# Optimization experiments

Hardware: AMD Instinct MI355X
Metric: run time of the kernel (lower is better)

## Reference

```python
import jax, jax.numpy as jnp
import numpy as np


def _freq_downsample(x, sf):
    # torch: stack(chunk(dim=2), 4) -> cat(chunk(dim=3), 4) -> mean(-1) -> repeat(1,1,sf,sf)
    # equivalent: mean over the sf x sf grid of contiguous blocks, then tile back.
    B, C, H, W = x.shape
    m = x.reshape(B, C, sf, H // sf, sf, W // sf).mean(axis=(2, 4))
    return jnp.tile(m, (1, 1, sf, sf))


def setup_inputs() -> dict:
    key = jax.random.key(0)
    k1, k2, k3 = jax.random.split(key, 3)
    shape = (4, 3, 256, 256)
    return {
        "STy": jax.random.normal(k1, shape, dtype=jnp.float32),
        "Fk_real": jax.random.normal(k2, shape, dtype=jnp.float32),
        "Fk_imag": jax.random.normal(k3, shape, dtype=jnp.float32),
        "sf": 2,
    }


def _forward(STy, Fk_real, Fk_imag, sf, num_iters=50, alpha=1e-6, gam=0.1):
    fft2 = lambda a: jnp.fft.fft2(a, axes=(-2, -1))
    ifft2 = lambda a: jnp.fft.ifft2(a, axes=(-2, -1))

    Fk = jax.lax.complex(Fk_real, Fk_imag)          # complex64 OTF
    FkC = jnp.conj(Fk)
    Fk2 = Fk_real ** 2 + Fk_imag ** 2               # |Fk|^2, real

    FSTy = fft2(STy)
    Fr = FkC * FSTy / (_freq_downsample(Fk2, sf) + alpha)
    pred = ifft2(Fr).real

    # finite-difference stencils DH = [1,-1] horizontal, DV vertical
    DH = jnp.zeros_like(pred).at[..., 0, 0].set(1.0).at[..., 0, 1].set(-1.0)
    DV = jnp.zeros_like(pred).at[..., 0, 0].set(1.0).at[..., 1, 0].set(-1.0)
    FDH, FDV = fft2(DH), fft2(DV)
    FDHC, FDVC = jnp.conj(FDH), jnp.conj(FDV)
    FD2 = jnp.abs(FDV) ** 2 + jnp.abs(FDH) ** 2 + 1e-8  # real

    # loop-invariant terms (identical math to recomputing each iteration)
    den = _freq_downsample(Fk2 / FD2, sf) + alpha
    FkFSTy = FkC * FSTy

    def body(carry, k):
        pred, x_old, t_old, U1, U2, D1, D2 = carry
        gam_k = gam * jnp.exp2(-k / num_iters)      # gam * 0.5 ** (k/num_iters)
        Fr = FkFSTy + alpha * (FDHC * fft2(U1 - D1) + FDVC * fft2(U2 - D2))
        Fr = (Fr - FkC * _freq_downsample(Fk * Fr / FD2, sf) / den) / (alpha * FD2)
        x_new = ifft2(Fr).real
        t_new = (1.0 + jnp.sqrt(1.0 + 4.0 * t_old ** 2)) / 2.0
        pred = x_new + (t_old - 1.0) / t_new * (x_new - x_old)
        DHr = ifft2(Fr * FDH).real
        DVr = ifft2(Fr * FDV).real
        NU1, NU2 = DHr + D1, DVr + D2
        NU = jnp.sqrt(NU1 ** 2 + NU2 ** 2 + 1e-8)
        A = jnp.maximum(0.0, NU - gam_k) + 1e-8
        A = A / (A + gam_k)                         # soft-threshold magnitude shrink
        U1n, U2n = A * NU1, A * NU2
        return (pred, x_new, t_new, U1n, U2n, D1 + DHr - U1n, D2 + DVr - U2n), None

    carry0 = (pred, pred, jnp.float32(1.0), pred, pred,
              jnp.zeros_like(pred), jnp.zeros_like(pred))
    ks = jnp.arange(num_iters, dtype=jnp.float32)
    (pred, *_), _ = jax.lax.scan(body, carry0, ks)
    return pred


def reference(STy, Fk_real, Fk_imag, sf):
    return _forward(STy, Fk_real, Fk_imag, sf)
```

## Files before the change

### kernel.cpp

```cpp
#include <hip/hip_runtime.h>
#include <math.h>

#define NIMG 12
#define NSZ 256
#define HWSZ 65536
#define NBLK 768

__device__ __forceinline__ float2 ld8(const float2* p)
{
  unsigned long long v = __hip_atomic_load((unsigned long long*)p, __ATOMIC_RELAXED,
                                           __HIP_MEMORY_SCOPE_AGENT);
  union { unsigned long long u; float2 f; } cv; cv.u = v; return cv.f;
}
__device__ __forceinline__ void st8(float2* p, float2 x)
{
  union { unsigned long long u; float2 f; } cv; cv.f = x;
  __hip_atomic_store((unsigned long long*)p, cv.u, __ATOMIC_RELAXED, __HIP_MEMORY_SCOPE_AGENT);
}
__device__ __forceinline__ float ld4(const float* p)
{
  unsigned v = __hip_atomic_load((unsigned*)p, __ATOMIC_RELAXED, __HIP_MEMORY_SCOPE_AGENT);
  union { unsigned u; float f; } cv; cv.u = v; return cv.f;
}
__device__ __forceinline__ void st4(float* p, float x)
{
  union { unsigned u; float f; } cv; cv.f = x;
  __hip_atomic_store((unsigned*)p, cv.u, __ATOMIC_RELAXED, __HIP_MEMORY_SCOPE_AGENT);
}

__device__ __forceinline__ size_t widx(int n, int u, int j)
{
  int tile = (j & 127) >> 1;
  int slot = (j & 1) + ((j >> 7) << 1);
  return ((((size_t)n << 6) + tile) << 10) + ((size_t)u << 2) + slot;
}

__device__ __forceinline__ void isync(unsigned* flags, int base, int sr, unsigned gen)
{
  asm volatile("s_waitcnt vmcnt(0)" ::: "memory");
  __syncthreads();
  int t = threadIdx.x;
  if (t < 64) {
    if (t == 0)
      __hip_atomic_store(&flags[base + sr], gen, __ATOMIC_RELAXED, __HIP_MEMORY_SCOPE_AGENT);
    unsigned v;
    int it = 0;
    do {
      if (it++ > 2) __builtin_amdgcn_s_sleep(2);
      v = __hip_atomic_load(&flags[base + t], __ATOMIC_RELAXED, __HIP_MEMORY_SCOPE_AGENT);
    } while (__any(v < gen));
  }
  __syncthreads();
  asm volatile("" ::: "memory");
}

__device__ __forceinline__ void r4_bfly(const float2* __restrict__ S, float2* __restrict__ D,
                                        int b, int m, float2 w1, float2 w2, float2 w3,
                                        float dir, bool usetw)
{
  int k = b & (m - 1);
  int base = ((b - k) << 2) + k;
  float2 x0 = S[b], x1 = S[b + 64], x2 = S[b + 128], x3 = S[b + 192];
  float t0x = x0.x + x2.x, t0y = x0.y + x2.y;
  float t1x = x0.x - x2.x, t1y = x0.y - x2.y;
  float t2x = x1.x + x3.x, t2y = x1.y + x3.y;
  float e3x = x1.x - x3.x, e3y = x1.y - x3.y;
  float t3x = -dir * e3y, t3y = dir * e3x;
  D[base] = make_float2(t0x + t2x, t0y + t2y);
  float y1x = t1x + t3x, y1y = t1y + t3y;
  float y2x = t0x - t2x, y2y = t0y - t2y;
  float y3x = t1x - t3x, y3y = t1y - t3y;
  if (usetw) {
    float w1i = dir * w1.y, w2i = dir * w2.y, w3i = dir * w3.y;
    D[base + m]     = make_float2(y1x * w1.x - y1y * w1i, y1x * w1i + y1y * w1.x);
    D[base + 2 * m] = make_float2(y2x * w2.x - y2y * w2i, y2x * w2i + y2y * w2.x);
    D[base + 3 * m] = make_float2(y3x * w3.x - y3y * w3i, y3x * w3i + y3y * w3.x);
  } else {
    D[base + m]     = make_float2(y1x, y1y);
    D[base + 2 * m] = make_float2(y2x, y2y);
    D[base + 3 * m] = make_float2(y3x, y3y);
  }
}

struct Tw { float2 a1, a2, a3, b1, b2, b3, c1, c2, c3; };

__device__ __forceinline__ float2 mktw(int q)
{
  float s, c;
  sincospif((float)q * (1.0f / 128.0f), &s, &c);
  return make_float2(c, s);
}

__device__ __forceinline__ void fft4_row(float2* A, float2* B, int lane, float dir, const Tw& tw)
{
  r4_bfly(A, B, lane, 1,  tw.a1, tw.a2, tw.a3, dir, true);
  r4_bfly(B, A, lane, 4,  tw.b1, tw.b2, tw.b3, dir, true);
  r4_bfly(A, B, lane, 16, tw.c1, tw.c2, tw.c3, dir, true);
  r4_bfly(B, A, lane, 64, tw.a1, tw.a1, tw.a1, dir, false);
}

__global__ __launch_bounds__(256, 3) void k_mega(const float* __restrict__ sty,
                                                 const float* __restrict__ fkr,
                                                 const float* __restrict__ fki,
                                                 float2* __restrict__ WG,
                                                 float2* __restrict__ WF,
                                                 float* __restrict__ Dh,
                                                 float* __restrict__ x49,
                                                 float* __restrict__ out,
                                                 float cmom, unsigned* flags)
{
  __shared__ __align__(16) float2 bufA[6][256];
  __shared__ __align__(16) float2 scrB[6][256];
  __shared__ float2 fkL[4][256];
  __shared__ float2 kfL[4][256];
  __shared__ float  dnL[256];
  __shared__ float  D1L[4][256];
  __shared__ float  D2L[4][256];

  float*   aL   = (float*)scrB;
  float*   bL   = ((float*)scrB) + 5 * 256;
  double2* Ml   = (double2*)scrB;
  float*   dsAp = (float*)scrB;

  int t = threadIdx.x;
  int slot = ((blockIdx.x & 7) * 96) + (blockIdx.x >> 3);
  int n = slot >> 6;
  int sr = slot & 63;
  int fbase = n << 6;
  int r0 = sr << 2;
  int j0 = sr << 1;
  int w = t >> 6, lane = t & 63;
  const float sc = 1.0f / 65536.0f;
  size_t cb = ((((size_t)n << 6) + sr) << 10);
  unsigned gen = 0;

  Tw tw;
  {
    int qa = lane, qb = lane & ~3, qc = lane & ~15;
    tw.a1 = mktw(qa);  tw.a2 = mktw(2 * qa); tw.a3 = mktw(3 * qa);
    tw.b1 = mktw(qb);  tw.b2 = mktw(2 * qb); tw.b3 = mktw(3 * qb);
    tw.c1 = mktw(qc);  tw.c2 = mktw(2 * qc); tw.c3 = mktw(3 * qc);
  }
  int u0 = t & 127, pp = t >> 7;
  double fdgc[4], rM[4], rF[4];
  double rdn0, rdn1;
  {
    double s;
    s = sinpi((double)u0 * (1.0 / 256.0));         double fdu0 = 4.0 * s * s;
    s = sinpi((double)(u0 + 128) * (1.0 / 256.0)); double fdu1 = 4.0 * s * s;
#pragma unroll
    for (int c = 0; c < 4; ++c) {
      int gc = j0 + (c & 1) + ((c >> 1) << 7);
      s = sinpi((double)gc * (1.0 / 256.0));
      fdgc[c] = 4.0 * s * s;
    }
#pragma unroll
    for (int s4 = 0; s4 < 4; ++s4) {
      double fdu = (s4 & 1) ? fdu1 : fdu0;
      rM[s4] = 1.0 / (fdu + fdgc[pp + ((s4 >> 1) << 1)] + 1e-8);
    }
    double fdt = pp ? fdu1 : fdu0;
#pragma unroll
    for (int c = 0; c < 4; ++c) rF[c] = 1.0 / (fdt + fdgc[c] + 1e-8);
  }

  {
    const float* src = sty + (size_t)n * HWSZ + (size_t)(r0 + w) * NSZ;
#pragma unroll
    for (int q = 0; q < 4; ++q) { int j = lane + (q << 6); bufA[w][j] = make_float2(src[j], 0.f); }
    fft4_row(bufA[w], scrB[w], lane, -1.f, tw);
#pragma unroll
    for (int q = 0; q < 4; ++q) { int j = lane + (q << 6); st8(&WG[widx(n, r0 + w, j)], bufA[w][j]); }
#pragma unroll
    for (int c = 0; c < 4; ++c) {
      int gc = j0 + (c & 1) + ((c >> 1) << 7);
      size_t idx = (size_t)n * HWSZ + (size_t)t * NSZ + gc;
      fkL[c][t] = make_float2(fkr[idx], fki[idx]);
    }
  }
  isync(flags, fbase, sr, ++gen);

  {
#pragma unroll
    for (int q = 0; q < 4; ++q) { int u = lane + (q << 6); bufA[w][u] = ld8(&WG[cb + (u << 2) + w]); }
    fft4_row(bufA[w], scrB[w], lane, -1.f, tw);
    __syncthreads();
#pragma unroll
    for (int c = 0; c < 4; ++c) {
      float2 K = fkL[c][t];
      float2 f = bufA[c][t];
      kfL[c][t] = make_float2(K.x * f.x + K.y * f.y, K.x * f.y - K.y * f.x);
    }
    {
      double s1 = 0.0, s2 = 0.0;
#pragma unroll
      for (int s4 = 0; s4 < 4; ++s4) {
        int u = u0 + ((s4 & 1) << 7);
        int c = pp + ((s4 >> 1) << 1);
        double kr = fkL[c][u].x, ki = fkL[c][u].y;
        double k2 = kr * kr + ki * ki;
        s1 += k2;
        s2 += k2 * rM[s4];
      }
      dnL[u0 * 2 + pp] = (float)(s2 * 0.25 + 1e-6);
      dsAp[pp * 128 + u0] = (float)(s1 * 0.25 + 1e-6);
    }
    __syncthreads();
    rdn0 = 1.0 / (double)dnL[u0 * 2];
    rdn1 = 1.0 / (double)dnL[u0 * 2 + 1];
#pragma unroll
    for (int c = 0; c < 4; ++c) {
      float d = dsAp[(c & 1) * 128 + u0];
      float2 kf = kfL[c][t];
      bufA[c][t] = make_float2(kf.x / d, kf.y / d);
    }
    __syncthreads();
    fft4_row(bufA[w], scrB[w], lane, +1.f, tw);
#pragma unroll
    for (int q = 0; q < 4; ++q) { int u = lane + (q << 6); st8(&WF[cb + (u << 2) + w], bufA[w][u]); }
  }
  isync(flags, fbase, sr, ++gen);

  for (int k = 0; k < 50; ++k) {
    float gamp = (k >= 1) ? (float)(0.1 * exp2(-(double)(k - 1) / 50.0)) : 0.f;

    {
      int gr = (r0 + w - 1) & 255;
#pragma unroll
      for (int q = 0; q < 4; ++q) { int j = lane + (q << 6); bufA[w][j] = ld8(&WF[widx(n, gr, j)]); }
      fft4_row(bufA[w], scrB[w], lane, +1.f, tw);
      if (w < 2) {
        int e = 4 + w;
        int gr2 = (r0 + e - 1) & 255;
#pragma unroll
        for (int q = 0; q < 4; ++q) { int j = lane + (q << 6); bufA[e][j] = ld8(&WF[widx(n, gr2, j)]); }
        fft4_row(bufA[e], scrB[e], lane, +1.f, tw);
      }
    }
    __syncthreads();
    {
      int jm1 = (t - 1) & 255;
      size_t hR = (((size_t)n << 6) + ((sr + 1) & 63)) << 9;
      size_t hW = (((size_t)n << 6) + sr) << 9;
      const float* DhP = Dh + (size_t)((k + 1) & 1) * (NBLK * 512);
      float* DhW = Dh + (size_t)(k & 1) * (NBLK * 512);
      for (int e = 1; e <= 5; ++e) {
        int gr = (r0 + e - 1) & 255;
        float xc = bufA[e][t].x * sc;
        if (k == 49 && e <= 4) x49[(size_t)n * HWSZ + (size_t)gr * NSZ + t] = xc;
        float a, b;
        if (k == 0) {
          a = xc; b = xc;
          if (e <= 4) { D1L[e - 1][t] = 0.f; D2L[e - 1][t] = 0.f; }
        } else {
          float dhr = xc - bufA[e][jm1].x * sc;
          float dvr = xc - bufA[e - 1][t].x * sc;
          float d1, d2;
          if (e <= 4) { d1 = D1L[e - 1][t]; d2 = D2L[e - 1][t]; }
          else        { d1 = ld4(&DhP[hR + t]); d2 = ld4(&DhP[hR + 256 + t]); }
          float nu1 = dhr + d1, nu2 = dvr + d2;
          float nu = sqrtf(nu1 * nu1 + nu2 * nu2 + 1e-8f);
          float A = fmaxf(0.f, nu - gamp) + 1e-8f;
          A = A / (A + gamp);
          float u1 = A * nu1, u2 = A * nu2;
          float d1v = d1 + dhr - u1;
          float d2v = d2 + dvr - u2;
          if (e <= 4) { D1L[e - 1][t] = d1v; D2L[e - 1][t] = d2v; }
          if (e == 1) { st4(&DhW[hW + t], d1v); st4(&DhW[hW + 256 + t], d2v); }
          a = u1 - d1v; b = u2 - d2v;
        }
        aL[(e - 1) * 256 + t] = a;
        bL[(e - 1) * 256 + t] = b;
      }
    }
    __syncthreads();
    {
#pragma unroll
      for (int q = 0; q < 4; ++q) {
        int j = lane + (q << 6);
        int jp1 = (j + 1) & 255;
        float g = aL[w * 256 + j] - aL[w * 256 + jp1] + bL[w * 256 + j] - bL[(w + 1) * 256 + j];
        bufA[w][j] = make_float2(g, 0.f);
      }
      fft4_row(bufA[w], scrB[w], lane, -1.f, tw);
#pragma unroll
      for (int q = 0; q < 4; ++q) { int j = lane + (q << 6); st8(&WG[widx(n, r0 + w, j)], bufA[w][j]); }
    }
    isync(flags, fbase, sr, ++gen);

    {
#pragma unroll
      for (int q = 0; q < 4; ++q) { int u = lane + (q << 6); bufA[w][u] = ld8(&WG[cb + (u << 2) + w]); }
      fft4_row(bufA[w], scrB[w], lane, -1.f, tw);
      __syncthreads();
#pragma unroll
      for (int c = 0; c < 4; ++c) {
        float2 kf = kfL[c][t];
        float2 fg = bufA[c][t];
        bufA[c][t] = make_float2(kf.x + 1e-6f * fg.x, kf.y + 1e-6f * fg.y);
      }
      __syncthreads();
      {
        double sx = 0.0, sy = 0.0;
#pragma unroll
        for (int s4 = 0; s4 < 4; ++s4) {
          int u = u0 + ((s4 & 1) << 7);
          int c = pp + ((s4 >> 1) << 1);
          float2 f1 = bufA[c][u];
          double kr = fkL[c][u].x, ki = fkL[c][u].y;
          sx += (kr * (double)f1.x - ki * (double)f1.y) * rM[s4];
          sy += (kr * (double)f1.y + ki * (double)f1.x) * rM[s4];
        }
        Ml[pp * 128 + u0] = make_double2(sx * 0.25, sy * 0.25);
      }
      __syncthreads();
#pragma unroll
      for (int c = 0; c < 4; ++c) {
        float2 f1 = bufA[c][t];
        double2 m = Ml[(c & 1) * 128 + u0];
        double rden = (c & 1) ? rdn1 : rdn0;
        double kr = fkL[c][t].x, ki = fkL[c][t].y;
        double px = (kr * m.x + ki * m.y) * rden;
        double py = (kr * m.y - ki * m.x) * rden;
        double s2 = 1e6 * rF[c];
        bufA[c][t] = make_float2((float)(((double)f1.x - px) * s2),
                                 (float)(((double)f1.y - py) * s2));
      }
      __syncthreads();
      fft4_row(bufA[w], scrB[w], lane, +1.f, tw);
#pragma unroll
      for (int q = 0; q < 4; ++q) { int u = lane + (q << 6); st8(&WF[cb + (u << 2) + w], bufA[w][u]); }
    }
    isync(flags, fbase, sr, ++gen);
  }

  {
    int gr = r0 + w;
#pragma unroll
    for (int q = 0; q < 4; ++q) { int j = lane + (q << 6); bufA[w][j] = ld8(&WF[widx(n, gr, j)]); }
    fft4_row(bufA[w], scrB[w], lane, +1.f, tw);
    size_t base = (size_t)n * HWSZ + (size_t)gr * NSZ;
#pragma unroll
    for (int q = 0; q < 4; ++q) {
      int j = lane + (q << 6);
      float v = bufA[w][j].x * sc;
      out[base + j] = v + cmom * (v - x49[base + j]);
    }
  }
}

__device__ __forceinline__ void fft256g(float2* A, float2* B, const float2* twl, int lane,
                                        float dir, bool active)
{
  float2* src = A;
  float2* dst = B;
  int m = 1;
#pragma unroll
  for (int s = 0; s < 8; ++s) {
    __syncthreads();
    if (active) {
#pragma unroll
      for (int h = 0; h < 2; ++h) {
        int b = lane + (h << 6);
        int k = b & (m - 1);
        int jm = b - k;
        float2 a = src[b];
        float2 c = src[b + 128];
        float2 wv = twl[jm];
        float wr = wv.x, wi = dir * wv.y;
        float ex = a.x - c.x, ey = a.y - c.y;
        dst[2 * jm + k]     = make_float2(a.x + c.x, a.y + c.y);
        dst[2 * jm + k + m] = make_float2(ex * wr - ey * wi, ex * wi + ey * wr);
      }
    }
    float2* t = src; src = dst; dst = t;
    m <<= 1;
  }
  __syncthreads();
}
__device__ __forceinline__ void fft256(float2* A, float2* B, const float2* twl, int lane, float dir)
{
  fft256g(A, B, twl, lane, dir, true);
}
__device__ __forceinline__ void make_tw(float2* twl, int t)
{
  float s, c;
  sincospif((float)t * (1.0f / 128.0f), &s, &c);
  twl[t] = make_float2(c, s);
}
__device__ __forceinline__ double fdval(const float2* twl, int k)
{
  return 2.0 - 2.0 * (double)twl[k].x;
}

__global__ __launch_bounds__(256) void k_rowfwd_sty(const float* __restrict__ sty,
                                                    float2* __restrict__ Wb)
{
  __shared__ float2 twl[256];
  __shared__ float2 bufA[4][256];
  __shared__ float2 bufB[4][256];
  int t = threadIdx.x;
  make_tw(twl, t);
  int n = blockIdx.x >> 6;
  int r0 = (blockIdx.x & 63) << 2;
  int w = t >> 6, lane = t & 63;
  const float* src = sty + (size_t)n * HWSZ + (size_t)(r0 + w) * NSZ;
#pragma unroll
  for (int q = 0; q < 4; ++q) { int j = lane + (q << 6); bufA[w][j] = make_float2(src[j], 0.f); }
  fft256(bufA[w], bufB[w], twl, lane, -1.f);
  float2* dst = Wb + (size_t)n * HWSZ + (size_t)(r0 + w) * NSZ;
#pragma unroll
  for (int q = 0; q < 4; ++q) { int j = lane + (q << 6); dst[j] = bufA[w][j]; }
}

__global__ __launch_bounds__(256) void k_colsetup(float2* __restrict__ Wb,
                                                  float2* __restrict__ FkF,
                                                  const float* __restrict__ fkr,
                                                  const float* __restrict__ fki,
                                                  float* __restrict__ denq)
{
  __shared__ float2 twl[256];
  __shared__ float2 bufA[4][256];
  __shared__ float2 bufB[4][256];
  __shared__ float dsA[2][128];
  int t = threadIdx.x;
  make_tw(twl, t);
  int n = blockIdx.x >> 6;
  int j0 = (blockIdx.x & 63) << 1;
  int w = t >> 6, lane = t & 63;
  int gcw = j0 + (w & 1) + ((w >> 1) << 7);
  float2* Wn = Wb + (size_t)n * HWSZ;
#pragma unroll
  for (int q = 0; q < 4; ++q) { int u = lane + (q << 6); bufA[w][u] = Wn[(size_t)u * NSZ + gcw]; }
  fft256(bufA[w], bufB[w], twl, lane, -1.f);
#pragma unroll
  for (int c = 0; c < 4; ++c) {
    int u = t;
    int gc = j0 + (c & 1) + ((c >> 1) << 7);
    size_t idx = (size_t)n * HWSZ + (size_t)u * NSZ + gc;
    float kr = fkr[idx], ki = fki[idx];
    float2 f = bufA[c][u];
    float2 kf = make_float2(kr * f.x + ki * f.y, kr * f.y - ki * f.x);
    FkF[idx] = kf;
    bufA[c][u] = kf;
  }
  __syncthreads();
  {
    int u0 = t & 127, p = t >> 7;
    double s1 = 0.0, s2 = 0.0;
#pragma unroll
    for (int s = 0; s < 4; ++s) {
      int u = u0 + ((s & 1) << 7);
      int c = p + ((s >> 1) << 1);
      int gc = j0 + (c & 1) + ((c >> 1) << 7);
      size_t idx = (size_t)n * HWSZ + (size_t)u * NSZ + gc;
      double kr = fkr[idx], ki = fki[idx];
      double k2 = kr * kr + ki * ki;
      double fd2 = fdval(twl, u) + fdval(twl, gc) + 1e-8;
      s1 += k2;
      s2 += k2 / fd2;
    }
    denq[(size_t)n * 16384 + (size_t)u0 * 128 + (j0 + p)] = (float)(s2 * 0.25 + 1e-6);
    dsA[p][u0] = (float)(s1 * 0.25 + 1e-6);
  }
  __syncthreads();
#pragma unroll
  for (int c = 0; c < 4; ++c) {
    int u = t;
    float d = dsA[c & 1][u & 127];
    float2 kf = bufA[c][u];
    bufA[c][u] = make_float2(kf.x / d, kf.y / d);
  }
  fft256(bufA[w], bufB[w], twl, lane, +1.f);
#pragma unroll
  for (int q = 0; q < 4; ++q) { int u = lane + (q << 6); Wn[(size_t)u * NSZ + gcw] = bufA[w][u]; }
}

__global__ __launch_bounds__(256) void k_spatial_rowfwd(const float* __restrict__ x,
                                                        const float* __restrict__ D1p,
                                                        const float* __restrict__ D2p,
                                                        float* __restrict__ D1n,
                                                        float* __restrict__ D2n,
                                                        float2* __restrict__ Wb,
                                                        float gamp, int firstIter)
{
  __shared__ float2 twl[256];
  __shared__ float aL[5][256];
  __shared__ float bL[5][256];
  __shared__ float2 bufA[4][256];
  __shared__ float2 bufB[4][256];
  int t = threadIdx.x;
  make_tw(twl, t);
  int n = blockIdx.x >> 6;
  int r0 = (blockIdx.x & 63) << 2;
  const float* xn = x + (size_t)n * HWSZ;
  for (int rr = 0; rr < 5; ++rr) {
    int i = (r0 + rr) & 255;
    int im1 = (i - 1) & 255;
    int j = t;
    int jm1 = (j - 1) & 255;
    float xc = xn[(size_t)i * NSZ + j];
    float a, b;
    if (firstIter) {
      a = xc; b = xc;
    } else {
      float dhr = xc - xn[(size_t)i * NSZ + jm1];
      float dvr = xc - xn[(size_t)im1 * NSZ + j];
      size_t idx = (size_t)n * HWSZ + (size_t)i * NSZ + j;
      float d1 = D1p[idx], d2 = D2p[idx];
      float nu1 = dhr + d1, nu2 = dvr + d2;
      float nu = sqrtf(nu1 * nu1 + nu2 * nu2 + 1e-8f);
      float A = fmaxf(0.f, nu - gamp) + 1e-8f;
      A = A / (A + gamp);
      float u1 = A * nu1, u2 = A * nu2;
      float d1v = d1 + dhr - u1;
      float d2v = d2 + dvr - u2;
      if (rr < 4) { D1n[idx] = d1v; D2n[idx] = d2v; }
      a = u1 - d1v; b = u2 - d2v;
    }
    aL[rr][j] = a;
    bL[rr][j] = b;
  }
  __syncthreads();
  int w = t >> 6, lane = t & 63;
#pragma unroll
  for (int q = 0; q < 4; ++q) {
    int j = lane + (q << 6);
    int jp1 = (j + 1) & 255;
    float g = aL[w][j] - aL[w][jp1] + bL[w][j] - bL[w + 1][j];
    bufA[w][j] = make_float2(g, 0.f);
  }
  fft256(bufA[w], bufB[w], twl, lane, -1.f);
  float2* dst = Wb + (size_t)n * HWSZ + (size_t)(r0 + w) * NSZ;
#pragma unroll
  for (int q = 0; q < 4; ++q) { int j = lane + (q << 6); dst[j] = bufA[w][j]; }
}

__global__ __launch_bounds__(256) void k_colphase(float2* __restrict__ Wb,
                                                  const float2* __restrict__ FkF,
                                                  const float* __restrict__ fkr,
                                                  const float* __restrict__ fki,
                                                  const float* __restrict__ denq)
{
  __shared__ float2 twl[256];
  __shared__ float2 bufA[4][256];
  __shared__ float2 bufB[4][256];
  __shared__ double2 Mll[2][128];
  int t = threadIdx.x;
  make_tw(twl, t);
  int n = blockIdx.x >> 6;
  int j0 = (blockIdx.x & 63) << 1;
  int w = t >> 6, lane = t & 63;
  int gcw = j0 + (w & 1) + ((w >> 1) << 7);
  float2* Wn = Wb + (size_t)n * HWSZ;
#pragma unroll
  for (int q = 0; q < 4; ++q) { int u = lane + (q << 6); bufA[w][u] = Wn[(size_t)u * NSZ + gcw]; }
  fft256(bufA[w], bufB[w], twl, lane, -1.f);
#pragma unroll
  for (int c = 0; c < 4; ++c) {
    int u = t;
    int gc = j0 + (c & 1) + ((c >> 1) << 7);
    size_t idx = (size_t)n * HWSZ + (size_t)u * NSZ + gc;
    float2 kf = FkF[idx];
    float2 fg = bufA[c][u];
    bufA[c][u] = make_float2(kf.x + 1e-6f * fg.x, kf.y + 1e-6f * fg.y);
  }
  __syncthreads();
  {
    int u0 = t & 127, p = t >> 7;
    double sx = 0.0, sy = 0.0;
#pragma unroll
    for (int s = 0; s < 4; ++s) {
      int u = u0 + ((s & 1) << 7);
      int c = p + ((s >> 1) << 1);
      int gc = j0 + (c & 1) + ((c >> 1) << 7);
      size_t idx = (size_t)n * HWSZ + (size_t)u * NSZ + gc;
      float2 f1 = bufA[c][u];
      double kr = fkr[idx], ki = fki[idx];
      double fd2 = fdval(twl, u) + fdval(twl, gc) + 1e-8;
      sx += (kr * (double)f1.x - ki * (double)f1.y) / fd2;
      sy += (kr * (double)f1.y + ki * (double)f1.x) / fd2;
    }
    Mll[p][u0] = make_double2(sx * 0.25, sy * 0.25);
  }
  __syncthreads();
#pragma unroll
  for (int c = 0; c < 4; ++c) {
    int u = t;
    int gc = j0 + (c & 1) + ((c >> 1) << 7);
    size_t idx = (size_t)n * HWSZ + (size_t)u * NSZ + gc;
    float2 f1 = bufA[c][u];
    double2 m = Mll[c & 1][u & 127];
    double den = (double)denq[(size_t)n * 16384 + (size_t)(u & 127) * 128 + (j0 + (c & 1))];
    double kr = fkr[idx], ki = fki[idx];
    double px = (kr * m.x + ki * m.y) / den;
    double py = (kr * m.y - ki * m.x) / den;
    double fd2 = fdval(twl, u) + fdval(twl, gc) + 1e-8;
    double s2 = 1.0 / (1e-6 * fd2);
    bufA[c][u] = make_float2((float)(((double)f1.x - px) * s2),
                             (float)(((double)f1.y - py) * s2));
  }
  fft256(bufA[w], bufB[w], twl, lane, +1.f);
#pragma unroll
  for (int q = 0; q < 4; ++q) { int u = lane + (q << 6); Wn[(size_t)u * NSZ + gcw] = bufA[w][u]; }
}

__global__ __launch_bounds__(256) void k_rowinv(const float2* __restrict__ Wb,
                                                float* __restrict__ xout,
                                                const float* __restrict__ xold,
                                                float* __restrict__ pred,
                                                float cmom, int isLast)
{
  __shared__ float2 twl[256];
  __shared__ float2 bufA[4][256];
  __shared__ float2 bufB[4][256];
  int t = threadIdx.x;
  make_tw(twl, t);
  int n = blockIdx.x >> 6;
  int r0 = (blockIdx.x & 63) << 2;
  int w = t >> 6, lane = t & 63;
  const float2* src = Wb + (size_t)n * HWSZ + (size_t)(r0 + w) * NSZ;
#pragma unroll
  for (int q = 0; q < 4; ++q) { int j = lane + (q << 6); bufA[w][j] = src[j]; }
  fft256(bufA[w], bufB[w], twl, lane, +1.f);
  size_t base = (size_t)n * HWSZ + (size_t)(r0 + w) * NSZ;
#pragma unroll
  for (int q = 0; q < 4; ++q) {
    int j = lane + (q << 6);
    float v = bufA[w][j].x * (1.0f / 65536.0f);
    xout[base + j] = v;
    if (isLast) pred[base + j] = v + cmom * (v - xold[base + j]);
  }
}

extern "C" void kernel_launch(void* const* d_in, const int* in_sizes, int n_in,
                              void* d_out, int out_size, void* d_ws, size_t ws_size,
                              hipStream_t stream)
{
  (void)in_sizes; (void)n_in; (void)out_size; (void)ws_size;
  const float* STy = (const float*)d_in[0];
  const float* fkr = (const float*)d_in[1];
  const float* fki = (const float*)d_in[2];
  float* out = (float*)d_out;

  char* p = (char*)d_ws;
  const size_t cplx = (size_t)NIMG * HWSZ * sizeof(float2);
  const size_t realb = (size_t)NIMG * HWSZ * sizeof(float);
  float2* WG  = (float2*)p; p += cplx;
  float2* WF  = (float2*)p; p += cplx;
  float2* FkF = (float2*)p; p += cplx;
  float* denq = (float*)p;  p += (size_t)NIMG * 16384 * sizeof(float);
  float* D1a = (float*)p;   p += realb;
  float* D2a = (float*)p;   p += realb;
  float* D1b = (float*)p;   p += realb;
  float* D2b = (float*)p;   p += realb;
  float* xA  = (float*)p;   p += realb;
  float* xB  = (float*)p;   p += realb;
  float* Dh  = (float*)p;   p += (size_t)2 * NBLK * 512 * sizeof(float);
  unsigned* flags = (unsigned*)p; p += 4096;

  double t_old = 1.0, cm = 0.0;
  for (int k = 0; k < 50; ++k) {
    double t_new = (1.0 + sqrt(1.0 + 4.0 * t_old * t_old)) * 0.5;
    if (k == 49) cm = (t_old - 1.0) / t_new;
    t_old = t_new;
  }

  int maxb = 0;
  hipError_t oe = hipOccupancyMaxActiveBlocksPerMultiprocessor(&maxb, k_mega, 256, 0);
  bool coop = (oe == hipSuccess && maxb >= 3);

  dim3 grid(NBLK), blk(256);
  if (coop) {
    hipMemsetAsync(Dh, 0, (size_t)2 * NBLK * 512 * sizeof(float), stream);
    hipMemsetAsync(flags, 0, 4096, stream);
    k_mega<<<grid, blk, 0, stream>>>(STy, fkr, fki, WG, WF, Dh, xA, out, (float)cm, flags);
  } else {
    hipMemsetAsync(D1a, 0, 2 * realb, stream);
    float2* Wb = WG;
    float* x0 = xA; float* x1 = xB;
    k_rowfwd_sty<<<grid, blk, 0, stream>>>(STy, Wb);
    k_colsetup<<<grid, blk, 0, stream>>>(Wb, FkF, fkr, fki, denq);
    k_rowinv<<<grid, blk, 0, stream>>>(Wb, x0, x0, out, 0.f, 0);
    double to = 1.0;
    for (int k = 0; k < 50; ++k) {
      float gamp = (k >= 1) ? (float)(0.1 * exp2(-(double)(k - 1) / 50.0)) : 0.f;
      const float* xk = (k & 1) ? x1 : x0;
      float* xn = (k & 1) ? x0 : x1;
      const float* D1p = (k & 1) ? D1a : D1b;
      const float* D2p = (k & 1) ? D2a : D2b;
      float* D1w = (k & 1) ? D1b : D1a;
      float* D2w = (k & 1) ? D2b : D2a;
      k_spatial_rowfwd<<<grid, blk, 0, stream>>>(xk, D1p, D2p, D1w, D2w, Wb, gamp, (k == 0) ? 1 : 0);
      k_colphase<<<grid, blk, 0, stream>>>(Wb, FkF, fkr, fki, denq);
      double tn = (1.0 + sqrt(1.0 + 4.0 * to * to)) * 0.5;
      int isLast = (k == 49) ? 1 : 0;
      float cmom = (float)((to - 1.0) / tn);
      k_rowinv<<<grid, blk, 0, stream>>>(Wb, xn, xk, out, isLast ? cmom : 0.f, isLast);
      to = tn;
    }
  }
}
```

Baseline: 2.494 ms.

## Pack real-signal row FFTs in pairs and pad sync flags to separate lines

Row inverse FFTs of real outputs are now computed two at a time by packing two rows into one complex transform (a + i·b), so three waves handle six rows instead of six separate transforms. The forward row FFTs of the real gradient field are likewise paired, and the two spectra are separated using conjugate symmetry. Each sync flag is also padded to its own 128-byte slot so that blocks polling flags do not contend on shared cache lines. In exchange, fewer waves are active during the FFT phases and there is some extra arithmetic and shared-memory traffic to unpack the two spectra.

```diff
diff --git a/kernel.cpp b/kernel.cpp
--- a/kernel.cpp
+++ b/kernel.cpp
@@ -35,19 +35,21 @@
   return ((((size_t)n << 6) + tile) << 10) + ((size_t)u << 2) + slot;
 }
 
-__device__ __forceinline__ void isync(unsigned* flags, int base, int sr, unsigned gen)
+__device__ __forceinline__ void isync(unsigned* flags, int fbase, int sr, unsigned gen)
 {
   asm volatile("s_waitcnt vmcnt(0)" ::: "memory");
   __syncthreads();
   int t = threadIdx.x;
   if (t < 64) {
     if (t == 0)
-      __hip_atomic_store(&flags[base + sr], gen, __ATOMIC_RELAXED, __HIP_MEMORY_SCOPE_AGENT);
+      __hip_atomic_store(&flags[(unsigned)(fbase + sr) << 5], gen, __ATOMIC_RELAXED,
+                         __HIP_MEMORY_SCOPE_AGENT);
     unsigned v;
     int it = 0;
     do {
       if (it++ > 2) __builtin_amdgcn_s_sleep(2);
-      v = __hip_atomic_load(&flags[base + t], __ATOMIC_RELAXED, __HIP_MEMORY_SCOPE_AGENT);
+      v = __hip_atomic_load(&flags[(unsigned)(fbase + t) << 5], __ATOMIC_RELAXED,
+                            __HIP_MEMORY_SCOPE_AGENT);
     } while (__any(v < gen));
   }
   __syncthreads();
@@ -109,18 +111,17 @@
                                                  float* __restrict__ out,
                                                  float cmom, unsigned* flags)
 {
-  __shared__ __align__(16) float2 bufA[6][256];
-  __shared__ __align__(16) float2 scrB[6][256];
+  __shared__ __align__(16) float2 xw[6][256];
+  __shared__ __align__(16) float2 sw[6][256];
   __shared__ float2 fkL[4][256];
   __shared__ float2 kfL[4][256];
   __shared__ float  dnL[256];
   __shared__ float  D1L[4][256];
   __shared__ float  D2L[4][256];
 
-  float*   aL   = (float*)scrB;
-  float*   bL   = ((float*)scrB) + 5 * 256;
-  double2* Ml   = (double2*)scrB;
-  float*   dsAp = (float*)scrB;
+  float*   swf  = (float*)sw;
+  double2* Ml   = (double2*)sw;
+  float*   dsAp = (float*)sw;
 
   int t = threadIdx.x;
   int slot = ((blockIdx.x & 7) * 96) + (blockIdx.x >> 3);
@@ -167,10 +168,10 @@
   {
     const float* src = sty + (size_t)n * HWSZ + (size_t)(r0 + w) * NSZ;
 #pragma unroll
-    for (int q = 0; q < 4; ++q) { int j = lane + (q << 6); bufA[w][j] = make_float2(src[j], 0.f); }
-    fft4_row(bufA[w], scrB[w], lane, -1.f, tw);
-#pragma unroll
-    for (int q = 0; q < 4; ++q) { int j = lane + (q << 6); st8(&WG[widx(n, r0 + w, j)], bufA[w][j]); }
+    for (int q = 0; q < 4; ++q) { int j = lane + (q << 6); xw[w][j] = make_float2(src[j], 0.f); }
+    fft4_row(xw[w], sw[w], lane, -1.f, tw);
+#pragma unroll
+    for (int q = 0; q < 4; ++q) { int j = lane + (q << 6); st8(&WG[widx(n, r0 + w, j)], xw[w][j]); }
 #pragma unroll
     for (int c = 0; c < 4; ++c) {
       int gc = j0 + (c & 1) + ((c >> 1) << 7);
@@ -182,13 +183,13 @@
 
   {
 #pragma unroll
-    for (int q = 0; q < 4; ++q) { int u = lane + (q << 6); bufA[w][u] = ld8(&WG[cb + (u << 2) + w]); }
-    fft4_row(bufA[w], scrB[w], lane, -1.f, tw);
+    for (int q = 0; q < 4; ++q) { int u = lane + (q << 6); xw[w][u] = ld8(&WG[cb + (u << 2) + w]); }
+    fft4_row(xw[w], sw[w], lane, -1.f, tw);
     __syncthreads();
 #pragma unroll
     for (int c = 0; c < 4; ++c) {
       float2 K = fkL[c][t];
-      float2 f = bufA[c][t];
+      float2 f = xw[c][t];
       kfL[c][t] = make_float2(K.x * f.x + K.y * f.y, K.x * f.y - K.y * f.x);
     }
     {
@@ -212,33 +213,34 @@
     for (int c = 0; c < 4; ++c) {
       float d = dsAp[(c & 1) * 128 + u0];
       float2 kf = kfL[c][t];
-      bufA[c][t] = make_float2(kf.x / d, kf.y / d);
+      xw[c][t] = make_float2(kf.x / d, kf.y / d);
     }
     __syncthreads();
-    fft4_row(bufA[w], scrB[w], lane, +1.f, tw);
-#pragma unroll
-    for (int q = 0; q < 4; ++q) { int u = lane + (q << 6); st8(&WF[cb + (u << 2) + w], bufA[w][u]); }
+    fft4_row(xw[w], sw[w], lane, +1.f, tw);
+#pragma unroll
+    for (int q = 0; q < 4; ++q) { int u = lane + (q << 6); st8(&WF[cb + (u << 2) + w], xw[w][u]); }
   }
   isync(flags, fbase, sr, ++gen);
 
   for (int k = 0; k < 50; ++k) {
     float gamp = (k >= 1) ? (float)(0.1 * exp2(-(double)(k - 1) / 50.0)) : 0.f;
 
-    {
-      int gr = (r0 + w - 1) & 255;
-#pragma unroll
-      for (int q = 0; q < 4; ++q) { int j = lane + (q << 6); bufA[w][j] = ld8(&WF[widx(n, gr, j)]); }
-      fft4_row(bufA[w], scrB[w], lane, +1.f, tw);
-      if (w < 2) {
-        int e = 4 + w;
-        int gr2 = (r0 + e - 1) & 255;
-#pragma unroll
-        for (int q = 0; q < 4; ++q) { int j = lane + (q << 6); bufA[e][j] = ld8(&WF[widx(n, gr2, j)]); }
-        fft4_row(bufA[e], scrB[e], lane, +1.f, tw);
-      }
+    if (w < 3) {
+      int grA = (r0 + 2 * w - 1) & 255;
+      int grB = (r0 + 2 * w) & 255;
+#pragma unroll
+      for (int q = 0; q < 4; ++q) {
+        int j = lane + (q << 6);
+        float2 a = ld8(&WF[widx(n, grA, j)]);
+        float2 b = ld8(&WF[widx(n, grB, j)]);
+        xw[w][j] = make_float2(a.x - b.y, a.y + b.x);
+      }
+      fft4_row(xw[w], sw[w + 3], lane, +1.f, tw);
     }
     __syncthreads();
     {
+      float* aL = swf;
+      float* bL = swf + 1280;
       int jm1 = (t - 1) & 255;
       size_t hR = (((size_t)n << 6) + ((sr + 1) & 63)) << 9;
       size_t hW = (((size_t)n << 6) + sr) << 9;
@@ -246,15 +248,20 @@
       float* DhW = Dh + (size_t)(k & 1) * (NBLK * 512);
       for (int e = 1; e <= 5; ++e) {
         int gr = (r0 + e - 1) & 255;
-        float xc = bufA[e][t].x * sc;
+        float2 pc = xw[e >> 1][t];
+        float xc = ((e & 1) ? pc.y : pc.x) * sc;
         if (k == 49 && e <= 4) x49[(size_t)n * HWSZ + (size_t)gr * NSZ + t] = xc;
         float a, b;
         if (k == 0) {
           a = xc; b = xc;
           if (e <= 4) { D1L[e - 1][t] = 0.f; D2L[e - 1][t] = 0.f; }
         } else {
-          float dhr = xc - bufA[e][jm1].x * sc;
-          float dvr = xc - bufA[e - 1][t].x * sc;
+          float2 pl = xw[e >> 1][jm1];
+          float xl = ((e & 1) ? pl.y : pl.x) * sc;
+          float2 pu = xw[(e - 1) >> 1][t];
+          float xu = (((e - 1) & 1) ? pu.y : pu.x) * sc;
+          float dhr = xc - xl;
+          float dvr = xc - xu;
           float d1, d2;
           if (e <= 4) { d1 = D1L[e - 1][t]; d2 = D2L[e - 1][t]; }
           else        { d1 = ld4(&DhP[hR + t]); d2 = ld4(&DhP[hR + 256 + t]); }
@@ -274,30 +281,43 @@
       }
     }
     __syncthreads();
-    {
+    if (w < 2) {
+      float* aL = swf;
+      float* bL = swf + 1280;
+      int ra = 2 * w, rb = 2 * w + 1;
 #pragma unroll
       for (int q = 0; q < 4; ++q) {
         int j = lane + (q << 6);
         int jp1 = (j + 1) & 255;
-        float g = aL[w * 256 + j] - aL[w * 256 + jp1] + bL[w * 256 + j] - bL[(w + 1) * 256 + j];
-        bufA[w][j] = make_float2(g, 0.f);
-      }
-      fft4_row(bufA[w], scrB[w], lane, -1.f, tw);
-#pragma unroll
-      for (int q = 0; q < 4; ++q) { int j = lane + (q << 6); st8(&WG[widx(n, r0 + w, j)], bufA[w][j]); }
+        float g0 = aL[ra * 256 + j] - aL[ra * 256 + jp1] + bL[ra * 256 + j] - bL[(ra + 1) * 256 + j];
+        float g1 = aL[rb * 256 + j] - aL[rb * 256 + jp1] + bL[rb * 256 + j] - bL[(rb + 1) * 256 + j];
+        xw[w][j] = make_float2(g0, g1);
+      }
+      fft4_row(xw[w], xw[w + 2], lane, -1.f, tw);
+      int r1 = r0 + ra, r2 = r0 + rb;
+#pragma unroll
+      for (int q = 0; q < 4; ++q) {
+        int j = lane + (q << 6);
+        int jm = (256 - j) & 255;
+        float2 Zj = xw[w][j], Zm = xw[w][jm];
+        float2 A  = make_float2((Zj.x + Zm.x) * 0.5f, (Zj.y - Zm.y) * 0.5f);
+        float2 Bc = make_float2((Zj.y + Zm.y) * 0.5f, (Zm.x - Zj.x) * 0.5f);
+        st8(&WG[widx(n, r1, j)], A);
+        st8(&WG[widx(n, r2, j)], Bc);
+      }
     }
     isync(flags, fbase, sr, ++gen);
 
     {
 #pragma unroll
-      for (int q = 0; q < 4; ++q) { int u = lane + (q << 6); bufA[w][u] = ld8(&WG[cb + (u << 2) + w]); }
-      fft4_row(bufA[w], scrB[w], lane, -1.f, tw);
+      for (int q = 0; q < 4; ++q) { int u = lane + (q << 6); xw[w][u] = ld8(&WG[cb + (u << 2) + w]); }
+      fft4_row(xw[w], sw[w], lane, -1.f, tw);
       __syncthreads();
 #pragma unroll
       for (int c = 0; c < 4; ++c) {
         float2 kf = kfL[c][t];
-        float2 fg = bufA[c][t];
-        bufA[c][t] = make_float2(kf.x + 1e-6f * fg.x, kf.y + 1e-6f * fg.y);
+        float2 fg = xw[c][t];
+        xw[c][t] = make_float2(kf.x + 1e-6f * fg.x, kf.y + 1e-6f * fg.y);
       }
       __syncthreads();
       {
@@ -306,7 +326,7 @@
         for (int s4 = 0; s4 < 4; ++s4) {
           int u = u0 + ((s4 & 1) << 7);
           int c = pp + ((s4 >> 1) << 1);
-          float2 f1 = bufA[c][u];
+          float2 f1 = xw[c][u];
           double kr = fkL[c][u].x, ki = fkL[c][u].y;
           sx += (kr * (double)f1.x - ki * (double)f1.y) * rM[s4];
           sy += (kr * (double)f1.y + ki * (double)f1.x) * rM[s4];
@@ -316,20 +336,20 @@
       __syncthreads();
 #pragma unroll
       for (int c = 0; c < 4; ++c) {
-        float2 f1 = bufA[c][t];
+        float2 f1 = xw[c][t];
         double2 m = Ml[(c & 1) * 128 + u0];
         double rden = (c & 1) ? rdn1 : rdn0;
         double kr = fkL[c][t].x, ki = fkL[c][t].y;
         double px = (kr * m.x + ki * m.y) * rden;
         double py = (kr * m.y - ki * m.x) * rden;
         double s2 = 1e6 * rF[c];
-        bufA[c][t] = make_float2((float)(((double)f1.x - px) * s2),
-                                 (float)(((double)f1.y - py) * s2));
+        xw[c][t] = make_float2((float)(((double)f1.x - px) * s2),
+                               (float)(((double)f1.y - py) * s2));
       }
       __syncthreads();
-      fft4_row(bufA[w], scrB[w], lane, +1.f, tw);
-#pragma unroll
-      for (int q = 0; q < 4; ++q) { int u = lane + (q << 6); st8(&WF[cb + (u << 2) + w], bufA[w][u]); }
+      fft4_row(xw[w], sw[w], lane, +1.f, tw);
+#pragma unroll
+      for (int q = 0; q < 4; ++q) { int u = lane + (q << 6); st8(&WF[cb + (u << 2) + w], xw[w][u]); }
     }
     isync(flags, fbase, sr, ++gen);
   }
@@ -337,13 +357,13 @@
   {
     int gr = r0 + w;
 #pragma unroll
-    for (int q = 0; q < 4; ++q) { int j = lane + (q << 6); bufA[w][j] = ld8(&WF[widx(n, gr, j)]); }
-    fft4_row(bufA[w], scrB[w], lane, +1.f, tw);
+    for (int q = 0; q < 4; ++q) { int j = lane + (q << 6); xw[w][j] = ld8(&WF[widx(n, gr, j)]); }
+    fft4_row(xw[w], sw[w], lane, +1.f, tw);
     size_t base = (size_t)n * HWSZ + (size_t)gr * NSZ;
 #pragma unroll
     for (int q = 0; q < 4; ++q) {
       int j = lane + (q << 6);
-      float v = bufA[w][j].x * sc;
+      float v = xw[w][j].x * sc;
       out[base + j] = v + cmom * (v - x49[base + j]);
     }
   }
@@ -657,7 +677,7 @@
   float* xA  = (float*)p;   p += realb;
   float* xB  = (float*)p;   p += realb;
   float* Dh  = (float*)p;   p += (size_t)2 * NBLK * 512 * sizeof(float);
-  unsigned* flags = (unsigned*)p; p += 4096;
+  unsigned* flags = (unsigned*)p; p += (size_t)NBLK * 32 * sizeof(unsigned);
 
   double t_old = 1.0, cm = 0.0;
   for (int k = 0; k < 50; ++k) {
@@ -673,7 +693,7 @@
   dim3 grid(NBLK), blk(256);
   if (coop) {
     hipMemsetAsync(Dh, 0, (size_t)2 * NBLK * 512 * sizeof(float), stream);
-    hipMemsetAsync(flags, 0, 4096, stream);
+    hipMemsetAsync(flags, 0, (size_t)NBLK * 32 * sizeof(unsigned), stream);
     k_mega<<<grid, blk, 0, stream>>>(STy, fkr, fki, WG, WF, Dh, xA, out, (float)cm, flags);
   } else {
     hipMemsetAsync(D1a, 0, 2 * realb, stream);
```

New measurement: 2.492 ms. Within noise of the previous version (-0.1%).
